# Optimization experiments

Hardware: AMD Instinct MI355X
Metric: run time of the kernel (lower is better)

Reference implementation:

```python
import jax, jax.numpy as jnp
import numpy as np


def setup_inputs() -> dict:
    key = jax.random.key(0)
    kq, kk, kv = jax.random.split(key, 3)
    B, S, D = 4, 4096, 64
    q = jax.random.normal(kq, (B, S, D), dtype=jnp.float32)
    k = jax.random.normal(kk, (B, S, D), dtype=jnp.float32)
    v = jax.random.normal(kv, (B, S, D), dtype=jnp.float32)
    return {"q": q, "k": k, "v": v}


def reference(q, k, v):
    # Faithful math of the original blocked loop:
    #   output_i += exp(Q_i @ K_j^T) @ V_j, summed over all column blocks j
    # which is exactly unnormalized exponential attention:
    #   out = exp(Q K^T) V  (no 1/sqrt(d) scaling, no softmax normalization,
    #   no max-subtraction -- matching the source module's math).
    scores = jnp.einsum("bqd,bkd->bqk", q, k)  # [B, Sq, Sk]
    return jnp.einsum("bqk,bkd->bqd", jnp.exp(scores), v)  # [B, Sq, D]
```

## Files before the change

### kernel.cpp

```cpp
#include <hip/hip_runtime.h>


typedef short    s16x4 __attribute__((ext_vector_type(4)));
typedef short    s16x8 __attribute__((ext_vector_type(8)));
typedef _Float16 h16x8 __attribute__((ext_vector_type(8)));
typedef float    fx4   __attribute__((ext_vector_type(4)));
typedef float    fx16  __attribute__((ext_vector_type(16)));

constexpr int S = 4096, D = 64, BQ = 64, BN = 128;
constexpr int TILES = S / BN;
constexpr int TILE_SHORTS  = 16 * 512;
constexpr int BATCH_SHORTS = TILES * TILE_SHORTS;

__device__ __forceinline__ unsigned short f2bf(float x) {
    unsigned u = __float_as_uint(x);
    u = (u + 0x7FFFu + ((u >> 16) & 1u)) >> 16;
    return (unsigned short)u;
}
__device__ __forceinline__ float bf2f(unsigned short h) {
    return __uint_as_float(((unsigned)h) << 16);
}
__device__ __forceinline__ unsigned short f2h(float x) {
    union { _Float16 h; unsigned short s; } u;
    u.h = (_Float16)x;
    return u.s;
}

__global__ __launch_bounds__(256) void prep2(
    const float* __restrict__ k, const float* __restrict__ v,
    unsigned short* __restrict__ kf, unsigned short* __restrict__ vf)
{
    __shared__ unsigned short tile[128 * 72];
    const int tid   = threadIdx.x;
    const int which = blockIdx.x & 1;
    const int t     = (blockIdx.x >> 1) & 31;
    const int b     = blockIdx.x >> 6;
    const float* src = (which ? v : k) + ((size_t)b * S + t * BN) * D;

    #pragma unroll
    for (int i = 0; i < 8; ++i) {
        int f   = i * 256 + tid;
        int row = f >> 4;
        int c4  = (f & 15) << 2;
        float4 x = *(const float4*)(src + row * D + c4);
        s16x4 o;
        if (which) o = (s16x4){(short)f2bf(x.x), (short)f2bf(x.y),
                               (short)f2bf(x.z), (short)f2bf(x.w)};
        else       o = (s16x4){(short)f2h(x.x), (short)f2h(x.y),
                               (short)f2h(x.z), (short)f2h(x.w)};
        *(s16x4*)&tile[row * 72 + c4] = o;
    }
    __syncthreads();

    const int lane = tid & 63;
    unsigned short* dst = (which ? vf : kf) + (size_t)b * BATCH_SHORTS + t * TILE_SHORTS;
    #pragma unroll
    for (int i = 0; i < 4; ++i) {
        int c = (tid >> 6) * 4 + i;
        s16x8 o;
        if (which == 0) {
            int row = (c >> 2) * 32 + (lane & 31);
            int dc  = (c & 3) * 16 + (lane >> 5) * 8;
            o = *(const s16x8*)&tile[row * 72 + dc];
        } else {
            int r0 = (c >> 1) * 16 + (lane >> 5) * 8;
            int dc = (c & 1) * 32 + (lane & 31);
            #pragma unroll
            for (int j = 0; j < 8; ++j) o[j] = (short)tile[(r0 + j) * 72 + dc];
        }
        *(s16x8*)(dst + c * 512 + lane * 8) = o;
    }
}

__global__ __launch_bounds__(512) void attn_main2(
    const float* __restrict__ q, const unsigned short* __restrict__ kf,
    const unsigned short* __restrict__ vf, float* __restrict__ out)
{
    __shared__ unsigned short smem[3 * 2 * TILE_SHORTS];

    const int tid = threadIdx.x, lane = tid & 63, w = tid >> 6;
    const int h = lane >> 5, m5 = lane & 31;
    const int mt = w & 1, kkq = w >> 1;
    const int b = blockIdx.y, q0 = blockIdx.x * BQ;

    const unsigned short* kfb = kf + (size_t)b * BATCH_SHORTS;
    const unsigned short* vfb = vf + (size_t)b * BATCH_SHORTS;

    h16x8 qf[4];
    {
        const float* qrow = q + ((size_t)b * S + q0 + mt * 32 + m5) * D + h * 8;
        #pragma unroll
        for (int ks = 0; ks < 4; ++ks) {
            float4 a = *(const float4*)(qrow + ks * 16);
            float4 c = *(const float4*)(qrow + ks * 16 + 4);
            qf[ks] = (h16x8){(_Float16)a.x, (_Float16)a.y, (_Float16)a.z, (_Float16)a.w,
                             (_Float16)c.x, (_Float16)c.y, (_Float16)c.z, (_Float16)c.w};
        }
    }

    fx16 oacc[2] = {};

    auto issue = [&](int t, int bi) {
        unsigned short* base = &smem[bi * 2 * TILE_SHORTS];
        #pragma unroll
        for (int ii = 0; ii < 4; ++ii) {
            int c = (ii & 1) * 8 + w;
            const unsigned short* g = (ii < 2 ? kfb : vfb)
                + (size_t)t * TILE_SHORTS + c * 512 + lane * 8;
            unsigned short* l = base + (ii < 2 ? 0 : TILE_SHORTS) + c * 512 + lane * 8;
            __builtin_amdgcn_global_load_lds(
                (const __attribute__((address_space(1))) unsigned int*)g,
                (__attribute__((address_space(3))) unsigned int*)l, 16, 0, 0);
        }
    };

    issue(0, 0);
    issue(1, 1);

    for (int t = 0; t < TILES; ++t) {
        const int bi = t % 3;
        __asm__ volatile("" ::: "memory");
        __builtin_amdgcn_s_waitcnt(0x0F74);
        __builtin_amdgcn_s_barrier();
        __asm__ volatile("" ::: "memory");
        issue((t + 2) & (TILES - 1), (t + 2) % 3);

        const unsigned short* kb = &smem[bi * 2 * TILE_SHORTS];
        const unsigned short* vb = kb + TILE_SHORTS;

        fx16 sa = {};
        #pragma unroll
        for (int ks = 0; ks < 4; ++ks) {
            h16x8 a = *(const h16x8*)(kb + (kkq * 4 + ks) * 512 + lane * 8);
            sa = __builtin_amdgcn_mfma_f32_32x32x16_f16(a, qf[ks], sa, 0, 0, 0);
        }

        unsigned p01[8], sw[8];
        #pragma unroll
        for (int r = 0; r < 8; ++r) {
            unsigned lo = f2bf(__expf(sa[2 * r]));
            unsigned hi = f2bf(__expf(sa[2 * r + 1]));
            p01[r] = lo | (hi << 16);
        }
        #pragma unroll
        for (int r = 0; r < 8; ++r) sw[r] = (unsigned)__shfl_xor((int)p01[r], 32, 64);

        union { unsigned u[4]; s16x8 v; } A1u, A2u;
        A1u.u[0] = h ? sw[2]  : p01[0];  A1u.u[1] = h ? sw[3]  : p01[1];
        A1u.u[2] = h ? p01[2] : sw[0];   A1u.u[3] = h ? p01[3] : sw[1];
        A2u.u[0] = h ? sw[6]  : p01[4];  A2u.u[1] = h ? sw[7]  : p01[5];
        A2u.u[2] = h ? p01[6] : sw[4];   A2u.u[3] = h ? p01[7] : sw[5];

        #pragma unroll
        for (int u = 0; u < 2; ++u) {
            s16x8 Au = u ? A2u.v : A1u.v;
            int ss = kkq * 2 + u;
            #pragma unroll
            for (int dt = 0; dt < 2; ++dt) {
                s16x8 vv = *(const s16x8*)(vb + (ss * 2 + dt) * 512 + lane * 8);
                oacc[dt] = __builtin_amdgcn_mfma_f32_32x32x16_bf16(Au, vv, oacc[dt], 0, 0, 0);
            }
        }
    }

    __syncthreads();
    float* scratch = (float*)smem;
    if (kkq > 0) {
        float* dst = scratch + (size_t)(mt * 3 + (kkq - 1)) * 2048;
        #pragma unroll
        for (int dt = 0; dt < 2; ++dt)
            #pragma unroll
            for (int r = 0; r < 16; ++r)
                dst[(dt * 16 + r) * 64 + lane] = oacc[dt][r];
    }
    __syncthreads();
    if (kkq == 0) {
        float* ob = out + (size_t)b * S * D;
        #pragma unroll
        for (int dt = 0; dt < 2; ++dt)
            #pragma unroll
            for (int r = 0; r < 16; ++r) {
                float val = oacc[dt][r];
                #pragma unroll
                for (int p = 0; p < 3; ++p)
                    val += scratch[(size_t)(mt * 3 + p) * 2048 + (dt * 16 + r) * 64 + lane];
                int row = q0 + mt * 32 + (r & 3) + 8 * (r >> 2) + 4 * h;
                ob[(size_t)row * D + dt * 32 + m5] = val;
            }
    }
}

__global__ __launch_bounds__(1024) void attn_fallback(
    const float* __restrict__ q, const float* __restrict__ k,
    const float* __restrict__ v, float* __restrict__ out)
{
    __shared__ unsigned short Kh[64][72];
    __shared__ unsigned short Kl[64][72];
    __shared__ unsigned short Vt[64][68];
    __shared__ unsigned short Pf[64][72];

    const int tid = threadIdx.x, lane = tid & 63, wave = tid >> 6;
    const int quad = lane >> 4, tq = lane & 15;
    const int kkb = wave & 3, mba = wave >> 2;
    const int b = blockIdx.y, q0 = blockIdx.x * 64;
    const float* qb = q + (size_t)b * S * D;
    const float* kb = k + (size_t)b * S * D;
    const float* vb = v + (size_t)b * S * D;
    float* ob = out + (size_t)b * S * D;

    s16x8 qh[2], ql[2];
    {
        const float* qrow = qb + (size_t)(q0 + mba * 16 + tq) * D;
        #pragma unroll
        for (int ks = 0; ks < 2; ++ks) {
            const float* src = qrow + ks * 32 + quad * 8;
            float4 f0 = *(const float4*)src;
            float4 f1 = *(const float4*)(src + 4);
            float f[8] = {f0.x, f0.y, f0.z, f0.w, f1.x, f1.y, f1.z, f1.w};
            #pragma unroll
            for (int j = 0; j < 8; ++j) {
                unsigned short hh = f2bf(f[j]);
                qh[ks][j] = (short)hh;
                ql[ks][j] = (short)f2bf(f[j] - bf2f(hh));
            }
        }
    }
    fx4 oacc = {0.f, 0.f, 0.f, 0.f};
    const int krow = tid >> 4, kc4 = (tid & 15) << 2;
    const int vd = tid & 63, vk = (tid >> 6) << 2;

    for (int t = 0; t < S / 64; ++t) {
        __syncthreads();
        const float* kt = kb + (size_t)(t * 64 + krow) * D;
        const float* vt = vb + (size_t)(t * 64 + vk) * D;
        {
            float4 kv = *(const float4*)(kt + kc4);
            unsigned short h0 = f2bf(kv.x), h1 = f2bf(kv.y), h2 = f2bf(kv.z), h3 = f2bf(kv.w);
            s16x4 a = {(short)h0, (short)h1, (short)h2, (short)h3};
            s16x4 l4 = {(short)f2bf(kv.x - bf2f(h0)), (short)f2bf(kv.y - bf2f(h1)),
                        (short)f2bf(kv.z - bf2f(h2)), (short)f2bf(kv.w - bf2f(h3))};
            *(s16x4*)&Kh[krow][kc4] = a;
            *(s16x4*)&Kl[krow][kc4] = l4;
            const float* vs = vt + vd;
            s16x4 vv = {(short)f2bf(vs[0]), (short)f2bf(vs[D]),
                        (short)f2bf(vs[2 * D]), (short)f2bf(vs[3 * D])};
            *(s16x4*)&Vt[vd][vk] = vv;
        }
        __syncthreads();
        fx4 sacc = {0.f, 0.f, 0.f, 0.f};
        #pragma unroll
        for (int ks = 0; ks < 2; ++ks) {
            s16x8 kah = *(const s16x8*)&Kh[kkb * 16 + tq][ks * 32 + quad * 8];
            s16x8 kal = *(const s16x8*)&Kl[kkb * 16 + tq][ks * 32 + quad * 8];
            sacc = __builtin_amdgcn_mfma_f32_16x16x32_bf16(kah, qh[ks], sacc, 0, 0, 0);
            sacc = __builtin_amdgcn_mfma_f32_16x16x32_bf16(kah, ql[ks], sacc, 0, 0, 0);
            sacc = __builtin_amdgcn_mfma_f32_16x16x32_bf16(kal, qh[ks], sacc, 0, 0, 0);
        }
        s16x4 pp = {(short)f2bf(__expf(sacc[0])), (short)f2bf(__expf(sacc[1])),
                    (short)f2bf(__expf(sacc[2])), (short)f2bf(__expf(sacc[3]))};
        *(s16x4*)&Pf[mba * 16 + tq][kkb * 16 + (quad << 2)] = pp;
        __syncthreads();
        #pragma unroll
        for (int ks = 0; ks < 2; ++ks) {
            s16x8 pa = *(const s16x8*)&Pf[mba * 16 + tq][ks * 32 + quad * 8];
            const unsigned short* vr = &Vt[kkb * 16 + tq][ks * 32 + quad * 8];
            s16x4 va = *(const s16x4*)vr;
            s16x4 vb2 = *(const s16x4*)(vr + 4);
            s16x8 vfull = __builtin_shufflevector(va, vb2, 0, 1, 2, 3, 4, 5, 6, 7);
            oacc = __builtin_amdgcn_mfma_f32_16x16x32_bf16(pa, vfull, oacc, 0, 0, 0);
        }
    }
    #pragma unroll
    for (int r = 0; r < 4; ++r)
        ob[(size_t)(q0 + mba * 16 + quad * 4 + r) * D + kkb * 16 + tq] = oacc[r];
}

extern "C" void kernel_launch(void* const* d_in, const int* in_sizes, int n_in,
                              void* d_out, int out_size, void* d_ws, size_t ws_size,
                              hipStream_t stream) {
    const float* q = (const float*)d_in[0];
    const float* k = (const float*)d_in[1];
    const float* v = (const float*)d_in[2];
    float* out = (float*)d_out;
    const int nbatch = in_sizes[0] / (S * D);

    const size_t need = (size_t)nbatch * S * D * 2 * 2;
    if (nbatch == 4 && ws_size >= need && d_ws != nullptr) {
        unsigned short* kf = (unsigned short*)d_ws;
        unsigned short* vf = kf + (size_t)nbatch * S * D;
        prep2<<<nbatch * TILES * 2, 256, 0, stream>>>(k, v, kf, vf);
        dim3 grid(S / BQ, nbatch);
        attn_main2<<<grid, 512, 0, stream>>>(q, kf, vf, out);
    } else {
        dim3 grid(S / 64, nbatch);
        attn_fallback<<<grid, 1024, 0, stream>>>(q, k, v, out);
    }
}
```

Baseline: 98.01 us.

## Split key dimension across two blocks with partial outputs and reduction kernel

Splits the key/value tiles into two halves along a new grid z dimension, so twice as many blocks run, each covering half the sequence. Each half writes a partial output to workspace and a new reduce kernel sums the two halves. The per-block pipeline drops from triple to double buffering, which shrinks LDS use so more blocks can be resident, and bf16 packing switches to the HIP intrinsic. The cost is an extra kernel launch plus partial-buffer traffic, and the double buffer gives less prefetch lead time per tile.

```diff
diff --git a/kernel.cpp b/kernel.cpp
--- a/kernel.cpp
+++ b/kernel.cpp
@@ -1,4 +1,5 @@
 #include <hip/hip_runtime.h>
+#include <hip/hip_bf16.h>
 
 
 typedef short    s16x4 __attribute__((ext_vector_type(4)));
@@ -9,6 +10,7 @@
 
 constexpr int S = 4096, D = 64, BQ = 64, BN = 128;
 constexpr int TILES = S / BN;
+constexpr int HALF_TILES = TILES / 2;
 constexpr int TILE_SHORTS  = 16 * 512;
 constexpr int BATCH_SHORTS = TILES * TILE_SHORTS;
 
@@ -24,6 +26,12 @@
     union { _Float16 h; unsigned short s; } u;
     u.h = (_Float16)x;
     return u.s;
+}
+__device__ __forceinline__ unsigned pack_bf16(float lo, float hi) {
+    __hip_bfloat162 r = __float22bfloat162_rn(make_float2(lo, hi));
+    union { __hip_bfloat162 b; unsigned u; } c;
+    c.b = r;
+    return c.u;
 }
 
 __global__ __launch_bounds__(256) void prep2(
@@ -72,16 +80,18 @@
     }
 }
 
-__global__ __launch_bounds__(512) void attn_main2(
+__global__ __launch_bounds__(512, 4) void attn_main3(
     const float* __restrict__ q, const unsigned short* __restrict__ kf,
-    const unsigned short* __restrict__ vf, float* __restrict__ out)
+    const unsigned short* __restrict__ vf, float* __restrict__ partial)
 {
-    __shared__ unsigned short smem[3 * 2 * TILE_SHORTS];
+    __shared__ unsigned short smem[2 * 2 * TILE_SHORTS];
 
     const int tid = threadIdx.x, lane = tid & 63, w = tid >> 6;
     const int h = lane >> 5, m5 = lane & 31;
     const int mt = w & 1, kkq = w >> 1;
     const int b = blockIdx.y, q0 = blockIdx.x * BQ;
+    const int kh = blockIdx.z;
+    const int t0 = kh * HALF_TILES;
 
     const unsigned short* kfb = kf + (size_t)b * BATCH_SHORTS;
     const unsigned short* vfb = vf + (size_t)b * BATCH_SHORTS;
@@ -114,16 +124,15 @@
         }
     };
 
-    issue(0, 0);
-    issue(1, 1);
-
-    for (int t = 0; t < TILES; ++t) {
-        const int bi = t % 3;
+    issue(t0, 0);
+
+    for (int i = 0; i < HALF_TILES; ++i) {
+        const int bi = i & 1;
         __asm__ volatile("" ::: "memory");
-        __builtin_amdgcn_s_waitcnt(0x0F74);
+        __builtin_amdgcn_s_waitcnt(0x0F70);
         __builtin_amdgcn_s_barrier();
         __asm__ volatile("" ::: "memory");
-        issue((t + 2) & (TILES - 1), (t + 2) % 3);
+        if (i + 1 < HALF_TILES) issue(t0 + i + 1, bi ^ 1);
 
         const unsigned short* kb = &smem[bi * 2 * TILE_SHORTS];
         const unsigned short* vb = kb + TILE_SHORTS;
@@ -137,11 +146,8 @@
 
         unsigned p01[8], sw[8];
         #pragma unroll
-        for (int r = 0; r < 8; ++r) {
-            unsigned lo = f2bf(__expf(sa[2 * r]));
-            unsigned hi = f2bf(__expf(sa[2 * r + 1]));
-            p01[r] = lo | (hi << 16);
-        }
+        for (int r = 0; r < 8; ++r)
+            p01[r] = pack_bf16(__expf(sa[2 * r]), __expf(sa[2 * r + 1]));
         #pragma unroll
         for (int r = 0; r < 8; ++r) sw[r] = (unsigned)__shfl_xor((int)p01[r], 32, 64);
 
@@ -175,7 +181,7 @@
     }
     __syncthreads();
     if (kkq == 0) {
-        float* ob = out + (size_t)b * S * D;
+        float* pout = partial + ((size_t)kh * gridDim.y + b) * S * D;
         #pragma unroll
         for (int dt = 0; dt < 2; ++dt)
             #pragma unroll
@@ -185,8 +191,19 @@
                 for (int p = 0; p < 3; ++p)
                     val += scratch[(size_t)(mt * 3 + p) * 2048 + (dt * 16 + r) * 64 + lane];
                 int row = q0 + mt * 32 + (r & 3) + 8 * (r >> 2) + 4 * h;
-                ob[(size_t)row * D + dt * 32 + m5] = val;
+                pout[(size_t)row * D + dt * 32 + m5] = val;
             }
+    }
+}
+
+__global__ __launch_bounds__(256) void reduce_out(
+    const float4* __restrict__ p0, const float4* __restrict__ p1,
+    float4* __restrict__ o, int n4)
+{
+    int i = blockIdx.x * 256 + threadIdx.x;
+    if (i < n4) {
+        float4 a = p0[i], b = p1[i];
+        o[i] = make_float4(a.x + b.x, a.y + b.y, a.z + b.z, a.w + b.w);
     }
 }
 
@@ -283,14 +300,21 @@
     const float* v = (const float*)d_in[2];
     float* out = (float*)d_out;
     const int nbatch = in_sizes[0] / (S * D);
-
-    const size_t need = (size_t)nbatch * S * D * 2 * 2;
+    const size_t elems = (size_t)nbatch * S * D;
+
+    const size_t need = elems * 2 * 2 + elems * 2 * 4;
     if (nbatch == 4 && ws_size >= need && d_ws != nullptr) {
         unsigned short* kf = (unsigned short*)d_ws;
-        unsigned short* vf = kf + (size_t)nbatch * S * D;
+        unsigned short* vf = kf + elems;
+        float* partial = (float*)(vf + elems);
+
         prep2<<<nbatch * TILES * 2, 256, 0, stream>>>(k, v, kf, vf);
-        dim3 grid(S / BQ, nbatch);
-        attn_main2<<<grid, 512, 0, stream>>>(q, kf, vf, out);
+        dim3 grid(S / BQ, nbatch, 2);
+        attn_main3<<<grid, 512, 0, stream>>>(q, kf, vf, partial);
+        const int n4 = (int)(elems / 4);
+        reduce_out<<<(n4 + 255) / 256, 256, 0, stream>>>(
+            (const float4*)partial, (const float4*)(partial + elems),
+            (float4*)out, n4);
     } else {
         dim3 grid(S / 64, nbatch);
         attn_fallback<<<grid, 1024, 0, stream>>>(q, k, v, out);
```

Result: no change. 96.99 us (-1.0%).

## Stream K/V fragments directly from global into registers, dropping LDS pipeline

Applied to the files above, without the earlier changes.

Replaces the triple-buffered global-to-LDS staging of K and V tiles with per-wave register double-buffering: each wave loads only its own K and V fragments straight from global memory, which removes the barriers and LDS traffic. Launch bounds now request two blocks per CU. On the bf16 P fragment path it uses permlane32_swap instead of shfl_xor plus selects, and a library bf16 pack instead of the manual rounding. The trade-off is that K/V data shared across the waves of a block is fetched redundantly through the cache hierarchy rather than once into LDS, and register pressure goes up.

```diff
diff --git a/kernel.cpp b/kernel.cpp
--- a/kernel.cpp
+++ b/kernel.cpp
@@ -1,4 +1,5 @@
 #include <hip/hip_runtime.h>
+#include <hip/hip_bf16.h>
 
 
 typedef short    s16x4 __attribute__((ext_vector_type(4)));
@@ -7,7 +8,7 @@
 typedef float    fx4   __attribute__((ext_vector_type(4)));
 typedef float    fx16  __attribute__((ext_vector_type(16)));
 
-constexpr int S = 4096, D = 64, BQ = 64, BN = 128;
+constexpr int S = 4096, D = 64, BN = 128;
 constexpr int TILES = S / BN;
 constexpr int TILE_SHORTS  = 16 * 512;
 constexpr int BATCH_SHORTS = TILES * TILE_SHORTS;
@@ -24,6 +25,17 @@
     union { _Float16 h; unsigned short s; } u;
     u.h = (_Float16)x;
     return u.s;
+}
+__device__ __forceinline__ unsigned pack_bf16(float lo, float hi) {
+    __hip_bfloat162 r = __float22bfloat162_rn(make_float2(lo, hi));
+    union { __hip_bfloat162 b; unsigned u; } c;
+    c.b = r;
+    return c.u;
+}
+__device__ __forceinline__ h16x8 as_h16(s16x8 x) {
+    union { s16x8 s; h16x8 h; } u;
+    u.s = x;
+    return u.h;
 }
 
 __global__ __launch_bounds__(256) void prep2(
@@ -72,19 +84,19 @@
     }
 }
 
-__global__ __launch_bounds__(512) void attn_main2(
+__global__ __launch_bounds__(512, 2) void attn_stream(
     const float* __restrict__ q, const unsigned short* __restrict__ kf,
     const unsigned short* __restrict__ vf, float* __restrict__ out)
 {
-    __shared__ unsigned short smem[3 * 2 * TILE_SHORTS];
+    __shared__ float scratch[6 * 2048];
 
     const int tid = threadIdx.x, lane = tid & 63, w = tid >> 6;
     const int h = lane >> 5, m5 = lane & 31;
     const int mt = w & 1, kkq = w >> 1;
-    const int b = blockIdx.y, q0 = blockIdx.x * BQ;
-
-    const unsigned short* kfb = kf + (size_t)b * BATCH_SHORTS;
-    const unsigned short* vfb = vf + (size_t)b * BATCH_SHORTS;
+    const int b = blockIdx.y, q0 = blockIdx.x * 64;
+
+    const unsigned short* kq = kf + (size_t)b * BATCH_SHORTS + (kkq * 4) * 512 + lane * 8;
+    const unsigned short* vq = vf + (size_t)b * BATCH_SHORTS + (kkq * 4) * 512 + lane * 8;
 
     h16x8 qf[4];
     {
@@ -100,71 +112,70 @@
 
     fx16 oacc[2] = {};
 
-    auto issue = [&](int t, int bi) {
-        unsigned short* base = &smem[bi * 2 * TILE_SHORTS];
-        #pragma unroll
-        for (int ii = 0; ii < 4; ++ii) {
-            int c = (ii & 1) * 8 + w;
-            const unsigned short* g = (ii < 2 ? kfb : vfb)
-                + (size_t)t * TILE_SHORTS + c * 512 + lane * 8;
-            unsigned short* l = base + (ii < 2 ? 0 : TILE_SHORTS) + c * 512 + lane * 8;
-            __builtin_amdgcn_global_load_lds(
-                (const __attribute__((address_space(1))) unsigned int*)g,
-                (__attribute__((address_space(3))) unsigned int*)l, 16, 0, 0);
+    s16x8 ka[4], va[4], kb[4], vb[4];
+
+    auto ldfrag = [&](int t, s16x8* kd, s16x8* vd) {
+        const size_t off = (size_t)t * TILE_SHORTS;
+        #pragma unroll
+        for (int i = 0; i < 4; ++i) {
+            kd[i] = *(const s16x8*)(kq + off + i * 512);
+            vd[i] = *(const s16x8*)(vq + off + i * 512);
         }
     };
 
-    issue(0, 0);
-    issue(1, 1);
-
-    for (int t = 0; t < TILES; ++t) {
-        const int bi = t % 3;
-        __asm__ volatile("" ::: "memory");
-        __builtin_amdgcn_s_waitcnt(0x0F74);
-        __builtin_amdgcn_s_barrier();
-        __asm__ volatile("" ::: "memory");
-        issue((t + 2) & (TILES - 1), (t + 2) % 3);
-
-        const unsigned short* kb = &smem[bi * 2 * TILE_SHORTS];
-        const unsigned short* vb = kb + TILE_SHORTS;
-
+    auto compute = [&](const s16x8* kc, const s16x8* vc) {
         fx16 sa = {};
         #pragma unroll
-        for (int ks = 0; ks < 4; ++ks) {
-            h16x8 a = *(const h16x8*)(kb + (kkq * 4 + ks) * 512 + lane * 8);
-            sa = __builtin_amdgcn_mfma_f32_32x32x16_f16(a, qf[ks], sa, 0, 0, 0);
-        }
-
-        unsigned p01[8], sw[8];
-        #pragma unroll
-        for (int r = 0; r < 8; ++r) {
-            unsigned lo = f2bf(__expf(sa[2 * r]));
-            unsigned hi = f2bf(__expf(sa[2 * r + 1]));
-            p01[r] = lo | (hi << 16);
-        }
-        #pragma unroll
-        for (int r = 0; r < 8; ++r) sw[r] = (unsigned)__shfl_xor((int)p01[r], 32, 64);
-
-        union { unsigned u[4]; s16x8 v; } A1u, A2u;
-        A1u.u[0] = h ? sw[2]  : p01[0];  A1u.u[1] = h ? sw[3]  : p01[1];
-        A1u.u[2] = h ? p01[2] : sw[0];   A1u.u[3] = h ? p01[3] : sw[1];
-        A2u.u[0] = h ? sw[6]  : p01[4];  A2u.u[1] = h ? sw[7]  : p01[5];
-        A2u.u[2] = h ? p01[6] : sw[4];   A2u.u[3] = h ? p01[7] : sw[5];
-
-        #pragma unroll
-        for (int u = 0; u < 2; ++u) {
-            s16x8 Au = u ? A2u.v : A1u.v;
-            int ss = kkq * 2 + u;
-            #pragma unroll
-            for (int dt = 0; dt < 2; ++dt) {
-                s16x8 vv = *(const s16x8*)(vb + (ss * 2 + dt) * 512 + lane * 8);
-                oacc[dt] = __builtin_amdgcn_mfma_f32_32x32x16_bf16(Au, vv, oacc[dt], 0, 0, 0);
-            }
-        }
-    }
-
-    __syncthreads();
-    float* scratch = (float*)smem;
+        for (int ks = 0; ks < 4; ++ks)
+            sa = __builtin_amdgcn_mfma_f32_32x32x16_f16(as_h16(kc[ks]), qf[ks], sa, 0, 0, 0);
+
+        unsigned p01[8];
+        #pragma unroll
+        for (int rp = 0; rp < 8; ++rp)
+            p01[rp] = pack_bf16(__expf(sa[2 * rp]), __expf(sa[2 * rp + 1]));
+
+        union frag { unsigned u[4]; s16x8 v; };
+        frag A[2];
+#if __has_builtin(__builtin_amdgcn_permlane32_swap)
+        typedef unsigned uix2 __attribute__((ext_vector_type(2)));
+        uix2 r0 = __builtin_amdgcn_permlane32_swap(p01[0], p01[2], false, false);
+        uix2 r1 = __builtin_amdgcn_permlane32_swap(p01[1], p01[3], false, false);
+        A[0].u[0] = r0.x; A[0].u[1] = r1.x; A[0].u[2] = r0.y; A[0].u[3] = r1.y;
+        uix2 r2 = __builtin_amdgcn_permlane32_swap(p01[4], p01[6], false, false);
+        uix2 r3 = __builtin_amdgcn_permlane32_swap(p01[5], p01[7], false, false);
+        A[1].u[0] = r2.x; A[1].u[1] = r3.x; A[1].u[2] = r2.y; A[1].u[3] = r3.y;
+#else
+        unsigned sw[8];
+        #pragma unroll
+        for (int rp = 0; rp < 8; ++rp)
+            sw[rp] = (unsigned)__shfl_xor((int)p01[rp], 32, 64);
+        A[0].u[0] = h ? sw[2]   : p01[0];
+        A[0].u[1] = h ? sw[3]   : p01[1];
+        A[0].u[2] = h ? p01[2]  : sw[0];
+        A[0].u[3] = h ? p01[3]  : sw[1];
+        A[1].u[0] = h ? sw[6]   : p01[4];
+        A[1].u[1] = h ? sw[7]   : p01[5];
+        A[1].u[2] = h ? p01[6]  : sw[4];
+        A[1].u[3] = h ? p01[7]  : sw[5];
+#endif
+
+        #pragma unroll
+        for (int u = 0; u < 2; ++u)
+            #pragma unroll
+            for (int dt = 0; dt < 2; ++dt)
+                oacc[dt] = __builtin_amdgcn_mfma_f32_32x32x16_bf16(
+                    A[u].v, vc[u * 2 + dt], oacc[dt], 0, 0, 0);
+    };
+
+    ldfrag(0, ka, va);
+    #pragma unroll 1
+    for (int t = 0; t < TILES; t += 2) {
+        ldfrag(t + 1, kb, vb);
+        compute(ka, va);
+        ldfrag((t + 2) & (TILES - 1), ka, va);
+        compute(kb, vb);
+    }
+
     if (kkq > 0) {
         float* dst = scratch + (size_t)(mt * 3 + (kkq - 1)) * 2048;
         #pragma unroll
@@ -283,14 +294,16 @@
     const float* v = (const float*)d_in[2];
     float* out = (float*)d_out;
     const int nbatch = in_sizes[0] / (S * D);
-
-    const size_t need = (size_t)nbatch * S * D * 2 * 2;
+    const size_t elems = (size_t)nbatch * S * D;
+
+    const size_t need = elems * 2 * 2;
     if (nbatch == 4 && ws_size >= need && d_ws != nullptr) {
         unsigned short* kf = (unsigned short*)d_ws;
-        unsigned short* vf = kf + (size_t)nbatch * S * D;
+        unsigned short* vf = kf + elems;
+
         prep2<<<nbatch * TILES * 2, 256, 0, stream>>>(k, v, kf, vf);
-        dim3 grid(S / BQ, nbatch);
-        attn_main2<<<grid, 512, 0, stream>>>(q, kf, vf, out);
+        dim3 grid(S / 64, nbatch);
+        attn_stream<<<grid, 512, 0, stream>>>(q, kf, vf, out);
     } else {
         dim3 grid(S / 64, nbatch);
         attn_fallback<<<grid, 1024, 0, stream>>>(q, k, v, out);
```

After: 94.38 us. 1.04x faster.
